# Optimization experiments

Hardware: AMD Instinct MI355X
Metric: run time of the kernel (lower is better)

Reference implementation:

```python
import jax, jax.numpy as jnp
import numpy as np

L_F, HOP, DELTA, L_S, COND, GH = 32, 16, 3, 96, 32, 64
B, T = 128, 48000


def setup_inputs() -> dict:
    key = jax.random.key(0)
    ks = jax.random.split(key, 12)
    s = 0.05
    return {
        "x": jax.random.normal(ks[0], (B, T), jnp.float32),
        # GRU (PyTorch layout): weight_ih (3H, L_S), weight_hh (3H, H)
        "W_ih": jax.random.normal(ks[1], (3 * GH, L_S), jnp.float32) * s,
        "W_hh": jax.random.normal(ks[2], (3 * GH, GH), jnp.float32) * s,
        "b_ih": jax.random.normal(ks[3], (3 * GH,), jnp.float32) * s,
        "b_hh": jax.random.normal(ks[4], (3 * GH,), jnp.float32) * s,
        # SlowBranch output projection -> cond_dim
        "W_cs": jax.random.normal(ks[5], (COND, GH), jnp.float32) * s,
        "b_cs": jax.random.normal(ks[6], (COND,), jnp.float32) * s,
        # FastEC MLP
        "W1": jax.random.normal(ks[7], (GH, L_F + COND), jnp.float32) * s,
        "b1": jax.random.normal(ks[8], (GH,), jnp.float32) * s,
        "W2": jax.random.normal(ks[9], (L_F, GH), jnp.float32) * s,
        "b2": jax.random.normal(ks[10], (L_F,), jnp.float32) * s,
    }


def reference(x, W_ih, W_hh, b_ih, b_hh, W_cs, b_cs, W1, b1, W2, b2):
    Bsz, Tlen = x.shape
    Nf = (Tlen - L_F) // HOP + 1
    win_s = DELTA * HOP * 2
    hop_s = DELTA * HOP
    Ns = (Tlen - win_s) // hop_s + 1

    f_starts = jnp.arange(Nf) * HOP                      # (Nf,)
    fast_idx = f_starts[:, None] + jnp.arange(L_F)       # (Nf, L_F)
    fast_frames = x[:, fast_idx]                         # (B, Nf, L_F)

    s_starts = jnp.arange(Ns) * hop_s
    slow_frames = x[:, s_starts[:, None] + jnp.arange(win_s)]  # (B, Ns, L_S)

    # Single-layer GRU over slow frames (PyTorch gate order r, z, n)
    def step(h, xt):
        gi = xt @ W_ih.T + b_ih                          # (B, 3H)
        gh = h @ W_hh.T + b_hh
        i_r, i_z, i_n = jnp.split(gi, 3, axis=-1)
        h_r, h_z, h_n = jnp.split(gh, 3, axis=-1)
        r = jax.nn.sigmoid(i_r + h_r)
        z = jax.nn.sigmoid(i_z + h_z)
        n = jnp.tanh(i_n + r * h_n)
        hn = (1.0 - z) * n + z * h
        return hn, hn

    h0 = jnp.zeros((Bsz, GH), x.dtype)
    _, hs = jax.lax.scan(step, h0, jnp.swapaxes(slow_frames, 0, 1))
    hs = jnp.swapaxes(hs, 0, 1)                          # (B, Ns, GH)
    c_s = hs @ W_cs.T + b_cs                             # (B, Ns, COND)

    # per-fast-frame conditioning vector (gather)
    idx = jnp.clip(jnp.arange(Nf) // DELTA - 1, 0, None)
    c = c_s[:, idx]                                      # (B, Nf, COND)

    # FastEC batched over all frames at once
    h = jnp.concatenate([fast_frames, c], axis=-1)       # (B, Nf, L_F+COND)
    h = jax.nn.relu(h @ W1.T + b1)
    y = h @ W2.T + b2                                    # (B, Nf, L_F)

    # overlap-add scatter
    out = jnp.zeros_like(x).at[:, fast_idx].add(y)
    return out
```

## Files before the change

kernel.cpp:

```cpp
#include <hip/hip_runtime.h>

constexpr int Bn  = 128;
constexpr int Tn  = 48000;
constexpr int NFn = 2999;
constexpr int NSn = 999;
constexpr int G3n = 192;
constexpr int GHn = 64;

typedef float f2 __attribute__((ext_vector_type(2)));

__global__ __launch_bounds__(192) void gi_kernel(const float* __restrict__ x,
                                                 const float* __restrict__ W_ih,
                                                 const float* __restrict__ b_ih,
                                                 float* __restrict__ GI) {
  __shared__ __align__(16) float WT[48 * 196];
  __shared__ float xs[1584];
  const int tile = blockIdx.x;
  const int b    = blockIdx.y;
  const int t0   = tile * 32;
  const int nt   = min(32, NSn - t0);
  const int tid  = threadIdx.x;

  const int span = (nt - 1) * 48 + 96;
  for (int i = tid; i < 1584; i += 192)
    xs[i] = (i < span) ? x[(size_t)b * Tn + t0 * 48 + i] : 0.0f;

  const int jq = tid % 48;
  const int tg = tid / 48;
  const int j0 = jq * 4;

  float acc[8][4];
#pragma unroll
  for (int u = 0; u < 8; ++u)
#pragma unroll
    for (int jj = 0; jj < 4; ++jj) acc[u][jj] = b_ih[j0 + jj];

  for (int half = 0; half < 2; ++half) {
    __syncthreads();
    for (int e = tid; e < 192 * 48; e += 192) {
      int j = e / 48, k = e % 48;
      WT[k * 196 + j] = W_ih[j * 96 + half * 48 + k];
    }
    __syncthreads();
    for (int k = 0; k < 48; ++k) {
      float4 w = *(const float4*)&WT[k * 196 + j0];
#pragma unroll
      for (int u = 0; u < 8; ++u) {
        float xv = xs[(tg * 8 + u) * 48 + half * 48 + k];
        acc[u][0] = fmaf(xv, w.x, acc[u][0]);
        acc[u][1] = fmaf(xv, w.y, acc[u][1]);
        acc[u][2] = fmaf(xv, w.z, acc[u][2]);
        acc[u][3] = fmaf(xv, w.w, acc[u][3]);
      }
    }
  }

#pragma unroll
  for (int u = 0; u < 8; ++u) {
    int tl = tg * 8 + u;
    if (tl < nt) {
      float4 st = make_float4(acc[u][0], acc[u][1], acc[u][2], acc[u][3]);
      *(float4*)&GI[(size_t)(b * NSn + t0 + tl) * G3n + j0] = st;
    }
  }
}

__device__ __forceinline__ float fsigmoid(float v) {
  return __fdividef(1.0f, 1.0f + __expf(-v));
}
__device__ __forceinline__ float ftanh_f(float v) {
  return 1.0f - __fdividef(2.0f, __expf(2.0f * v) + 1.0f);
}

__global__ __attribute__((amdgpu_flat_work_group_size(64, 64),
                          amdgpu_waves_per_eu(1, 1),
                          amdgpu_num_vgpr(256)))
void gru_kernel(const float* __restrict__ GI,
                const float* __restrict__ W_hh,
                const float* __restrict__ b_hh,
                float* __restrict__ hs) {
  __shared__ __align__(16) float hbuf[64];
  const int b = blockIdx.x;
  const int j = threadIdx.x;

  f2 wr2[32], wz2[32], wn2[32];
  const f2* Wr = (const f2*)(W_hh + (size_t)j * 64);
  const f2* Wz = (const f2*)(W_hh + (size_t)(j + 64) * 64);
  const f2* Wn = (const f2*)(W_hh + (size_t)(j + 128) * 64);
#pragma unroll
  for (int q = 0; q < 32; ++q) { wr2[q] = Wr[q]; wz2[q] = Wz[q]; wn2[q] = Wn[q]; }
#pragma unroll
  for (int q = 0; q < 32; ++q) {
    asm volatile("" : "+v"(wr2[q]));
    asm volatile("" : "+v"(wz2[q]));
    asm volatile("" : "+v"(wn2[q]));
  }
  const float br = b_hh[j], bz = b_hh[j + 64], bn = b_hh[j + 128];

  hbuf[j] = 0.0f;
  float hj = 0.0f;
  __builtin_amdgcn_wave_barrier();

  const float* gp = GI + (size_t)b * NSn * G3n;
  float* hsp = hs + (size_t)b * NSn * GHn;

  float pr0, pr1, pr2, pz0, pz1, pz2, pn0, pn1, pn2;
  pr0 = gp[0 * G3n + j];       pz0 = gp[0 * G3n + 64 + j];  pn0 = gp[0 * G3n + 128 + j];
  pr1 = gp[1 * G3n + j];       pz1 = gp[1 * G3n + 64 + j];  pn1 = gp[1 * G3n + 128 + j];

  for (int t = 0; t < NSn; ++t) {
    const size_t off = (size_t)min(t + 2, NSn - 1) * G3n;
    pr2 = gp[off + j];
    pz2 = gp[off + 64 + j];
    pn2 = gp[off + 128 + j];

    const f2* h2 = (const f2*)hbuf;
    f2 ar0 = {0.f, 0.f}, ar1 = {0.f, 0.f}, ar2 = {0.f, 0.f}, ar3 = {0.f, 0.f};
    f2 az0 = {0.f, 0.f}, az1 = {0.f, 0.f}, az2 = {0.f, 0.f}, az3 = {0.f, 0.f};
    f2 an0 = {0.f, 0.f}, an1 = {0.f, 0.f}, an2 = {0.f, 0.f}, an3 = {0.f, 0.f};
#pragma unroll
    for (int q = 0; q < 8; ++q) {
      f2 h0 = h2[q * 4 + 0], h1 = h2[q * 4 + 1], h2v = h2[q * 4 + 2], h3 = h2[q * 4 + 3];
      ar0 += wr2[q * 4 + 0] * h0; ar1 += wr2[q * 4 + 1] * h1;
      ar2 += wr2[q * 4 + 2] * h2v; ar3 += wr2[q * 4 + 3] * h3;
      az0 += wz2[q * 4 + 0] * h0; az1 += wz2[q * 4 + 1] * h1;
      az2 += wz2[q * 4 + 2] * h2v; az3 += wz2[q * 4 + 3] * h3;
      an0 += wn2[q * 4 + 0] * h0; an1 += wn2[q * 4 + 1] * h1;
      an2 += wn2[q * 4 + 2] * h2v; an3 += wn2[q * 4 + 3] * h3;
    }
    f2 sr = (ar0 + ar1) + (ar2 + ar3);
    f2 sz = (az0 + az1) + (az2 + az3);
    f2 sn = (an0 + an1) + (an2 + an3);

    float r = fsigmoid(pr0 + br + sr.x + sr.y);
    float z = fsigmoid(pz0 + bz + sz.x + sz.y);
    float n = ftanh_f(fmaf(r, bn + sn.x + sn.y, pn0));
    float hn = fmaf(z, hj - n, n);

    __builtin_amdgcn_wave_barrier();
    hbuf[j] = hn;
    __builtin_amdgcn_wave_barrier();
    hj = hn;
    hsp[(size_t)t * GHn + j] = hn;

    pr0 = pr1; pr1 = pr2;
    pz0 = pz1; pz1 = pz2;
    pn0 = pn1; pn1 = pn2;
  }
}

__global__ __launch_bounds__(256) void cs_kernel(const float* __restrict__ hs,
                                                 const float* __restrict__ W_cs,
                                                 const float* __restrict__ b_cs,
                                                 float* __restrict__ cs) {
  __shared__ __align__(16) float WcT[64 * 36];
  __shared__ __align__(16) float hsl[32 * 65];
  __shared__ __align__(16) float bcs[32];
  const int tile = blockIdx.x;
  const int b    = blockIdx.y;
  const int t0   = tile * 32;
  const int nt   = min(32, NSn - t0);
  const int tid  = threadIdx.x;

  for (int e = tid; e < 32 * 64; e += 256) {
    int i = e >> 6, k = e & 63;
    WcT[k * 36 + i] = W_cs[e];
  }
  for (int e = tid; e < nt * 64; e += 256) {
    int t = e >> 6, k = e & 63;
    hsl[t * 65 + k] = hs[((size_t)b * NSn + t0 + t) * GHn + k];
  }
  if (tid < 32) bcs[tid] = b_cs[tid];
  __syncthreads();

  const int oq = tid & 7;
  const int t  = tid >> 3;
  if (t < nt) {
    float4 acc = *(const float4*)&bcs[oq * 4];
    const float* hr = &hsl[t * 65];
#pragma unroll 4
    for (int k = 0; k < 64; ++k) {
      float hv = hr[k];
      float4 w = *(const float4*)&WcT[k * 36 + oq * 4];
      acc.x = fmaf(w.x, hv, acc.x);
      acc.y = fmaf(w.y, hv, acc.y);
      acc.z = fmaf(w.z, hv, acc.z);
      acc.w = fmaf(w.w, hv, acc.w);
    }
    *(float4*)&cs[((size_t)b * NSn + t0 + t) * 32 + oq * 4] = acc;
  }
}

__global__ __launch_bounds__(256) void out_kernel(const float* __restrict__ x,
                                                  const float* __restrict__ cs,
                                                  const float* __restrict__ W1,
                                                  const float* __restrict__ b1,
                                                  const float* __restrict__ W2,
                                                  const float* __restrict__ b2,
                                                  float* __restrict__ out) {
  __shared__ __align__(16) float A[33 * 65];
  __shared__ __align__(16) float W1T[64 * 68];
  __shared__ __align__(16) float W2T[64 * 36];
  __shared__ __align__(16) float h1loc[33 * 65];
  __shared__ __align__(16) float yloc[33 * 32];
  __shared__ __align__(16) float bb1[64];
  __shared__ __align__(16) float bb2[32];

  const int fb  = blockIdx.x;
  const int b   = blockIdx.y;
  const int f0  = fb * 32;
  const int nf  = min(33, NFn - f0);
  const int tid = threadIdx.x;

  for (int e = tid; e < 64 * 64; e += 256) {
    int o = e >> 6, k = e & 63;
    W1T[k * 68 + o] = W1[e];
  }
  for (int e = tid; e < 32 * 64; e += 256) {
    int o = e >> 6, k = e & 63;
    W2T[k * 36 + o] = W2[e];
  }
  if (tid < 64) bb1[tid] = b1[tid];
  if (tid < 32) bb2[tid] = b2[tid];

  for (int e = tid; e < 33 * 32; e += 256) {
    int lf = e >> 5, k = e & 31;
    int g = (f0 + lf) * 16 + k;
    A[lf * 65 + k] = (lf < nf && g < Tn) ? x[(size_t)b * Tn + g] : 0.0f;
  }
  for (int e = tid; e < 33 * 32; e += 256) {
    int lf = e >> 5, k = e & 31;
    int ts = max((f0 + lf) / 3 - 1, 0);
    A[lf * 65 + 32 + k] = (lf < nf) ? cs[((size_t)b * NSn + ts) * 32 + k] : 0.0f;
  }
  __syncthreads();

  for (int it = tid; it < 33 * 16; it += 256) {
    int lf = it >> 4, oq = it & 15;
    float4 acc = *(const float4*)&bb1[oq * 4];
    const float* ar = &A[lf * 65];
#pragma unroll 4
    for (int k = 0; k < 64; ++k) {
      float av = ar[k];
      float4 w = *(const float4*)&W1T[k * 68 + oq * 4];
      acc.x = fmaf(w.x, av, acc.x);
      acc.y = fmaf(w.y, av, acc.y);
      acc.z = fmaf(w.z, av, acc.z);
      acc.w = fmaf(w.w, av, acc.w);
    }
    acc.x = fmaxf(acc.x, 0.0f); acc.y = fmaxf(acc.y, 0.0f);
    acc.z = fmaxf(acc.z, 0.0f); acc.w = fmaxf(acc.w, 0.0f);
    *(float4*)&h1loc[lf * 65 + oq * 4] = acc;
  }
  __syncthreads();

  for (int it = tid; it < 33 * 8; it += 256) {
    int lf = it >> 3, oq = it & 7;
    float4 acc = *(const float4*)&bb2[oq * 4];
    const float* hr = &h1loc[lf * 65];
#pragma unroll 4
    for (int k = 0; k < 64; ++k) {
      float hv = hr[k];
      float4 w = *(const float4*)&W2T[k * 36 + oq * 4];
      acc.x = fmaf(w.x, hv, acc.x);
      acc.y = fmaf(w.y, hv, acc.y);
      acc.z = fmaf(w.z, hv, acc.z);
      acc.w = fmaf(w.w, hv, acc.w);
    }
    *(float4*)&yloc[lf * 32 + oq * 4] = acc;
  }
  __syncthreads();

  const int s0 = f0 * 16 + 16;
  const int s1 = min(s0 + 512, Tn);
  for (int s = s0 + tid; s < s1; s += 256) {
    int f1  = s >> 4;
    int o1  = s & 15;
    int lf1 = f1 - f0;
    float v = yloc[(lf1 - 1) * 32 + o1 + 16];
    if (lf1 < nf) v += yloc[lf1 * 32 + o1];
    out[(size_t)b * Tn + s] = v;
  }
  if (fb == 0 && tid < 16) out[(size_t)b * Tn + tid] = yloc[tid];
}

extern "C" void kernel_launch(void* const* d_in, const int* in_sizes, int n_in,
                              void* d_out, int out_size, void* d_ws, size_t ws_size,
                              hipStream_t stream) {
  const float* x    = (const float*)d_in[0];
  const float* W_ih = (const float*)d_in[1];
  const float* W_hh = (const float*)d_in[2];
  const float* b_ih = (const float*)d_in[3];
  const float* b_hh = (const float*)d_in[4];
  const float* W_cs = (const float*)d_in[5];
  const float* b_cs = (const float*)d_in[6];
  const float* W1   = (const float*)d_in[7];
  const float* b1   = (const float*)d_in[8];
  const float* W2   = (const float*)d_in[9];
  const float* b2   = (const float*)d_in[10];
  float* out = (float*)d_out;

  float* GI = (float*)d_ws;
  float* hs = GI + (size_t)Bn * NSn * G3n;
  float* cs = GI;

  gi_kernel<<<dim3(32, Bn), 192, 0, stream>>>(x, W_ih, b_ih, GI);
  gru_kernel<<<Bn, 64, 0, stream>>>(GI, W_hh, b_hh, hs);
  cs_kernel<<<dim3(32, Bn), 256, 0, stream>>>(hs, W_cs, b_cs, cs);
  out_kernel<<<dim3(94, Bn), 256, 0, stream>>>(x, cs, W1, b1, W2, b2, out);
}
```

Before: 875.7 us.

## Split GRU recurrence matvec across four waves with readlane broadcast and LDS reduction

The GRU kernel moves from one 64-thread wave per batch element to four waves, each covering a 16-wide slice of the hidden-state dot product. The hidden state is broadcast with readlane instead of a shared-memory round trip. Partial sums go through double-buffered LDS and are joined after a workgroup barrier. This cuts the serial FMA chain per timestep by four and frees registers, but adds a block-wide barrier and an LDS reduction to every step of the sequential loop.

```diff
diff --git a/kernel.cpp b/kernel.cpp
--- a/kernel.cpp
+++ b/kernel.cpp
@@ -8,6 +8,7 @@
 constexpr int GHn = 64;
 
 typedef float f2 __attribute__((ext_vector_type(2)));
+typedef float f4 __attribute__((ext_vector_type(4)));
 
 __global__ __launch_bounds__(192) void gi_kernel(const float* __restrict__ x,
                                                  const float* __restrict__ W_ih,
@@ -72,34 +73,38 @@
   return 1.0f - __fdividef(2.0f, __expf(2.0f * v) + 1.0f);
 }
 
-__global__ __attribute__((amdgpu_flat_work_group_size(64, 64),
-                          amdgpu_waves_per_eu(1, 1),
-                          amdgpu_num_vgpr(256)))
-void gru_kernel(const float* __restrict__ GI,
-                const float* __restrict__ W_hh,
-                const float* __restrict__ b_hh,
-                float* __restrict__ hs) {
-  __shared__ __align__(16) float hbuf[64];
-  const int b = blockIdx.x;
-  const int j = threadIdx.x;
-
-  f2 wr2[32], wz2[32], wn2[32];
-  const f2* Wr = (const f2*)(W_hh + (size_t)j * 64);
-  const f2* Wz = (const f2*)(W_hh + (size_t)(j + 64) * 64);
-  const f2* Wn = (const f2*)(W_hh + (size_t)(j + 128) * 64);
-#pragma unroll
-  for (int q = 0; q < 32; ++q) { wr2[q] = Wr[q]; wz2[q] = Wz[q]; wn2[q] = Wn[q]; }
-#pragma unroll
-  for (int q = 0; q < 32; ++q) {
-    asm volatile("" : "+v"(wr2[q]));
-    asm volatile("" : "+v"(wz2[q]));
-    asm volatile("" : "+v"(wn2[q]));
+#define GRU_LBAR()                                             \
+  do {                                                         \
+    asm volatile("s_waitcnt lgkmcnt(0)" ::: "memory");         \
+    __builtin_amdgcn_s_barrier();                              \
+    asm volatile("" ::: "memory");                             \
+  } while (0)
+
+__global__ __launch_bounds__(256) void gru_kernel(const float* __restrict__ GI,
+                                                  const float* __restrict__ W_hh,
+                                                  const float* __restrict__ b_hh,
+                                                  float* __restrict__ hs) {
+  __shared__ __align__(16) float parts[2][4][64][4];
+  const int tid = threadIdx.x;
+  const int wid = tid >> 6;
+  const int j   = tid & 63;
+  const int b   = blockIdx.x;
+  const int k0  = wid * 16;
+
+  f4 wr4[4], wz4[4], wn4[4];
+#pragma unroll
+  for (int q = 0; q < 4; ++q) {
+    wr4[q] = *(const f4*)&W_hh[(size_t)j * 64 + k0 + 4 * q];
+    wz4[q] = *(const f4*)&W_hh[(size_t)(j + 64) * 64 + k0 + 4 * q];
+    wn4[q] = *(const f4*)&W_hh[(size_t)(j + 128) * 64 + k0 + 4 * q];
+  }
+#pragma unroll
+  for (int q = 0; q < 4; ++q) {
+    asm volatile("" : "+v"(wr4[q]));
+    asm volatile("" : "+v"(wz4[q]));
+    asm volatile("" : "+v"(wn4[q]));
   }
   const float br = b_hh[j], bz = b_hh[j + 64], bn = b_hh[j + 128];
-
-  hbuf[j] = 0.0f;
-  float hj = 0.0f;
-  __builtin_amdgcn_wave_barrier();
 
   const float* gp = GI + (size_t)b * NSn * G3n;
   float* hsp = hs + (size_t)b * NSn * GHn;
@@ -107,6 +112,8 @@
   float pr0, pr1, pr2, pz0, pz1, pz2, pn0, pn1, pn2;
   pr0 = gp[0 * G3n + j];       pz0 = gp[0 * G3n + 64 + j];  pn0 = gp[0 * G3n + 128 + j];
   pr1 = gp[1 * G3n + j];       pz1 = gp[1 * G3n + 64 + j];  pn1 = gp[1 * G3n + 128 + j];
+
+  float hn = 0.0f;
 
   for (int t = 0; t < NSn; ++t) {
     const size_t off = (size_t)min(t + 2, NSn - 1) * G3n;
@@ -114,34 +121,49 @@
     pz2 = gp[off + 64 + j];
     pn2 = gp[off + 128 + j];
 
-    const f2* h2 = (const f2*)hbuf;
-    f2 ar0 = {0.f, 0.f}, ar1 = {0.f, 0.f}, ar2 = {0.f, 0.f}, ar3 = {0.f, 0.f};
-    f2 az0 = {0.f, 0.f}, az1 = {0.f, 0.f}, az2 = {0.f, 0.f}, az3 = {0.f, 0.f};
-    f2 an0 = {0.f, 0.f}, an1 = {0.f, 0.f}, an2 = {0.f, 0.f}, an3 = {0.f, 0.f};
-#pragma unroll
-    for (int q = 0; q < 8; ++q) {
-      f2 h0 = h2[q * 4 + 0], h1 = h2[q * 4 + 1], h2v = h2[q * 4 + 2], h3 = h2[q * 4 + 3];
-      ar0 += wr2[q * 4 + 0] * h0; ar1 += wr2[q * 4 + 1] * h1;
-      ar2 += wr2[q * 4 + 2] * h2v; ar3 += wr2[q * 4 + 3] * h3;
-      az0 += wz2[q * 4 + 0] * h0; az1 += wz2[q * 4 + 1] * h1;
-      az2 += wz2[q * 4 + 2] * h2v; az3 += wz2[q * 4 + 3] * h3;
-      an0 += wn2[q * 4 + 0] * h0; an1 += wn2[q * 4 + 1] * h1;
-      an2 += wn2[q * 4 + 2] * h2v; an3 += wn2[q * 4 + 3] * h3;
-    }
-    f2 sr = (ar0 + ar1) + (ar2 + ar3);
-    f2 sz = (az0 + az1) + (az2 + az3);
-    f2 sn = (an0 + an1) + (an2 + an3);
-
-    float r = fsigmoid(pr0 + br + sr.x + sr.y);
-    float z = fsigmoid(pz0 + bz + sz.x + sz.y);
-    float n = ftanh_f(fmaf(r, bn + sn.x + sn.y, pn0));
-    float hn = fmaf(z, hj - n, n);
-
-    __builtin_amdgcn_wave_barrier();
-    hbuf[j] = hn;
-    __builtin_amdgcn_wave_barrier();
-    hj = hn;
-    hsp[(size_t)t * GHn + j] = hn;
+    float sh[16];
+#pragma unroll
+    for (int m = 0; m < 16; ++m)
+      sh[m] = __uint_as_float(
+          __builtin_amdgcn_readlane(__float_as_uint(hn), k0 + m));
+
+    float ar0 = 0.f, ar1 = 0.f, ar2 = 0.f, ar3 = 0.f;
+    float az0 = 0.f, az1 = 0.f, az2 = 0.f, az3 = 0.f;
+    float an0 = 0.f, an1 = 0.f, an2 = 0.f, an3 = 0.f;
+#pragma unroll
+    for (int q = 0; q < 4; ++q) {
+      float h0 = sh[4 * q + 0], h1 = sh[4 * q + 1];
+      float h2v = sh[4 * q + 2], h3 = sh[4 * q + 3];
+      ar0 = fmaf(wr4[q][0], h0, ar0); ar1 = fmaf(wr4[q][1], h1, ar1);
+      ar2 = fmaf(wr4[q][2], h2v, ar2); ar3 = fmaf(wr4[q][3], h3, ar3);
+      az0 = fmaf(wz4[q][0], h0, az0); az1 = fmaf(wz4[q][1], h1, az1);
+      az2 = fmaf(wz4[q][2], h2v, az2); az3 = fmaf(wz4[q][3], h3, az3);
+      an0 = fmaf(wn4[q][0], h0, an0); an1 = fmaf(wn4[q][1], h1, an1);
+      an2 = fmaf(wn4[q][2], h2v, an2); an3 = fmaf(wn4[q][3], h3, an3);
+    }
+    f4 pv;
+    pv[0] = (ar0 + ar1) + (ar2 + ar3);
+    pv[1] = (az0 + az1) + (az2 + az3);
+    pv[2] = (an0 + an1) + (an2 + an3);
+    pv[3] = 0.f;
+    *(f4*)&parts[t & 1][wid][j][0] = pv;
+
+    GRU_LBAR();
+
+    const f4 p0 = *(const f4*)&parts[t & 1][0][j][0];
+    const f4 p1 = *(const f4*)&parts[t & 1][1][j][0];
+    const f4 p2 = *(const f4*)&parts[t & 1][2][j][0];
+    const f4 p3 = *(const f4*)&parts[t & 1][3][j][0];
+    float sr = (p0[0] + p1[0]) + (p2[0] + p3[0]);
+    float sz = (p0[1] + p1[1]) + (p2[1] + p3[1]);
+    float sn = (p0[2] + p1[2]) + (p2[2] + p3[2]);
+
+    float r = fsigmoid(pr0 + br + sr);
+    float z = fsigmoid(pz0 + bz + sz);
+    float n = ftanh_f(fmaf(r, bn + sn, pn0));
+    hn = fmaf(z, hn - n, n);
+
+    if (wid == 0) hsp[(size_t)t * GHn + j] = hn;
 
     pr0 = pr1; pr1 = pr2;
     pz0 = pz1; pz1 = pz2;
@@ -305,7 +327,7 @@
   float* cs = GI;
 
   gi_kernel<<<dim3(32, Bn), 192, 0, stream>>>(x, W_ih, b_ih, GI);
-  gru_kernel<<<Bn, 64, 0, stream>>>(GI, W_hh, b_hh, hs);
+  gru_kernel<<<Bn, 256, 0, stream>>>(GI, W_hh, b_hh, hs);
   cs_kernel<<<dim3(32, Bn), 256, 0, stream>>>(hs, W_cs, b_cs, cs);
   out_kernel<<<dim3(94, Bn), 256, 0, stream>>>(x, cs, W1, b1, W2, b2, out);
 }
```

Result: slower. 1.080 ms (+23.3%).

## Hold MLP weights in registers and split K across threads in out_kernel

Applied to the files above, without the earlier changes.

The FastEC MLP kernel stops staging transposed W1/W2 in shared memory. Each thread now loads a 4x32 slice of weights straight from global memory into registers and computes a half-K partial dot product for several frames. A shared-memory reduction then sums the two halves and applies the bias and ReLU. The aim is to cut LDS traffic and shared-memory weight loads, at the cost of very high register use (launch_bounds min-blocks 1), which may limit occupancy, plus extra syncs for the partial sums.

```diff
diff --git a/kernel.cpp b/kernel.cpp
--- a/kernel.cpp
+++ b/kernel.cpp
@@ -8,6 +8,7 @@
 constexpr int GHn = 64;
 
 typedef float f2 __attribute__((ext_vector_type(2)));
+typedef float f4 __attribute__((ext_vector_type(4)));
 
 __global__ __launch_bounds__(192) void gi_kernel(const float* __restrict__ x,
                                                  const float* __restrict__ W_ih,
@@ -191,17 +192,17 @@
   }
 }
 
-__global__ __launch_bounds__(256) void out_kernel(const float* __restrict__ x,
-                                                  const float* __restrict__ cs,
-                                                  const float* __restrict__ W1,
-                                                  const float* __restrict__ b1,
-                                                  const float* __restrict__ W2,
-                                                  const float* __restrict__ b2,
-                                                  float* __restrict__ out) {
-  __shared__ __align__(16) float A[33 * 65];
-  __shared__ __align__(16) float W1T[64 * 68];
-  __shared__ __align__(16) float W2T[64 * 36];
-  __shared__ __align__(16) float h1loc[33 * 65];
+__global__ __launch_bounds__(256, 1) void out_kernel(const float* __restrict__ x,
+                                                     const float* __restrict__ cs,
+                                                     const float* __restrict__ W1,
+                                                     const float* __restrict__ b1,
+                                                     const float* __restrict__ W2,
+                                                     const float* __restrict__ b2,
+                                                     float* __restrict__ out) {
+  __shared__ __align__(16) float A[33 * 68];
+  __shared__ __align__(16) float P[2][33][64];
+  __shared__ __align__(16) float h1loc[33 * 68];
+  __shared__ __align__(16) float P2[2][33][32];
   __shared__ __align__(16) float yloc[33 * 32];
   __shared__ __align__(16) float bb1[64];
   __shared__ __align__(16) float bb2[32];
@@ -212,62 +213,115 @@
   const int nf  = min(33, NFn - f0);
   const int tid = threadIdx.x;
 
-  for (int e = tid; e < 64 * 64; e += 256) {
-    int o = e >> 6, k = e & 63;
-    W1T[k * 68 + o] = W1[e];
-  }
-  for (int e = tid; e < 32 * 64; e += 256) {
-    int o = e >> 6, k = e & 63;
-    W2T[k * 36 + o] = W2[e];
-  }
+  const int oq  = tid & 15;
+  const int kh  = (tid >> 4) & 1;
+  const int lfp = tid >> 5;
+
+  f4 w1r[4][8];
+#pragma unroll
+  for (int r = 0; r < 4; ++r)
+#pragma unroll
+    for (int i = 0; i < 8; ++i)
+      w1r[r][i] = *(const f4*)&W1[(size_t)(oq * 4 + r) * 64 + kh * 32 + 4 * i];
+
   if (tid < 64) bb1[tid] = b1[tid];
   if (tid < 32) bb2[tid] = b2[tid];
 
   for (int e = tid; e < 33 * 32; e += 256) {
     int lf = e >> 5, k = e & 31;
     int g = (f0 + lf) * 16 + k;
-    A[lf * 65 + k] = (lf < nf && g < Tn) ? x[(size_t)b * Tn + g] : 0.0f;
+    A[lf * 68 + k] = (lf < nf && g < Tn) ? x[(size_t)b * Tn + g] : 0.0f;
   }
   for (int e = tid; e < 33 * 32; e += 256) {
     int lf = e >> 5, k = e & 31;
     int ts = max((f0 + lf) / 3 - 1, 0);
-    A[lf * 65 + 32 + k] = (lf < nf) ? cs[((size_t)b * NSn + ts) * 32 + k] : 0.0f;
-  }
-  __syncthreads();
-
-  for (int it = tid; it < 33 * 16; it += 256) {
-    int lf = it >> 4, oq = it & 15;
-    float4 acc = *(const float4*)&bb1[oq * 4];
-    const float* ar = &A[lf * 65];
-#pragma unroll 4
-    for (int k = 0; k < 64; ++k) {
-      float av = ar[k];
-      float4 w = *(const float4*)&W1T[k * 68 + oq * 4];
-      acc.x = fmaf(w.x, av, acc.x);
-      acc.y = fmaf(w.y, av, acc.y);
-      acc.z = fmaf(w.z, av, acc.z);
-      acc.w = fmaf(w.w, av, acc.w);
-    }
-    acc.x = fmaxf(acc.x, 0.0f); acc.y = fmaxf(acc.y, 0.0f);
-    acc.z = fmaxf(acc.z, 0.0f); acc.w = fmaxf(acc.w, 0.0f);
-    *(float4*)&h1loc[lf * 65 + oq * 4] = acc;
-  }
-  __syncthreads();
-
-  for (int it = tid; it < 33 * 8; it += 256) {
-    int lf = it >> 3, oq = it & 7;
-    float4 acc = *(const float4*)&bb2[oq * 4];
-    const float* hr = &h1loc[lf * 65];
-#pragma unroll 4
-    for (int k = 0; k < 64; ++k) {
-      float hv = hr[k];
-      float4 w = *(const float4*)&W2T[k * 36 + oq * 4];
-      acc.x = fmaf(w.x, hv, acc.x);
-      acc.y = fmaf(w.y, hv, acc.y);
-      acc.z = fmaf(w.z, hv, acc.z);
-      acc.w = fmaf(w.w, hv, acc.w);
-    }
-    *(float4*)&yloc[lf * 32 + oq * 4] = acc;
+    A[lf * 68 + 32 + k] = (lf < nf) ? cs[((size_t)b * NSn + ts) * 32 + k] : 0.0f;
+  }
+  __syncthreads();
+
+#pragma unroll
+  for (int m = 0; m < 5; ++m) {
+    const int lf = lfp + 8 * m;
+    if (lf < 33) {
+      const f4* ar = (const f4*)&A[lf * 68 + kh * 32];
+      f4 av[8];
+#pragma unroll
+      for (int i = 0; i < 8; ++i) av[i] = ar[i];
+      float a0 = 0.f, a1 = 0.f, a2 = 0.f, a3 = 0.f;
+#pragma unroll
+      for (int i = 0; i < 8; ++i) {
+#pragma unroll
+        for (int c = 0; c < 4; ++c) {
+          const float avc = av[i][c];
+          a0 = fmaf(w1r[0][i][c], avc, a0);
+          a1 = fmaf(w1r[1][i][c], avc, a1);
+          a2 = fmaf(w1r[2][i][c], avc, a2);
+          a3 = fmaf(w1r[3][i][c], avc, a3);
+        }
+      }
+      f4 pv = {a0, a1, a2, a3};
+      *(f4*)&P[kh][lf][oq * 4] = pv;
+    }
+  }
+  __syncthreads();
+
+  for (int e = tid; e < 33 * 16; e += 256) {
+    const int lf = e >> 4, q = e & 15;
+    f4 p0 = *(const f4*)&P[0][lf][q * 4];
+    f4 p1 = *(const f4*)&P[1][lf][q * 4];
+    f4 bq = *(const f4*)&bb1[q * 4];
+    f4 s = p0 + p1 + bq;
+#pragma unroll
+    for (int c = 0; c < 4; ++c) s[c] = fmaxf(s[c], 0.f);
+    *(f4*)&h1loc[lf * 68 + q * 4] = s;
+  }
+  __syncthreads();
+
+  const int oq2  = tid & 7;
+  const int kh2  = (tid >> 3) & 1;
+  const int lfp2 = tid >> 4;
+
+  asm volatile("" ::: "memory");
+  f4 w2r[4][8];
+#pragma unroll
+  for (int r = 0; r < 4; ++r)
+#pragma unroll
+    for (int i = 0; i < 8; ++i)
+      w2r[r][i] = *(const f4*)&W2[(size_t)(oq2 * 4 + r) * 64 + kh2 * 32 + 4 * i];
+
+#pragma unroll
+  for (int m = 0; m < 3; ++m) {
+    const int lf = lfp2 + 16 * m;
+    if (lf < 33) {
+      const f4* hr = (const f4*)&h1loc[lf * 68 + kh2 * 32];
+      f4 hv[8];
+#pragma unroll
+      for (int i = 0; i < 8; ++i) hv[i] = hr[i];
+      float a0 = 0.f, a1 = 0.f, a2 = 0.f, a3 = 0.f;
+#pragma unroll
+      for (int i = 0; i < 8; ++i) {
+#pragma unroll
+        for (int c = 0; c < 4; ++c) {
+          const float hvc = hv[i][c];
+          a0 = fmaf(w2r[0][i][c], hvc, a0);
+          a1 = fmaf(w2r[1][i][c], hvc, a1);
+          a2 = fmaf(w2r[2][i][c], hvc, a2);
+          a3 = fmaf(w2r[3][i][c], hvc, a3);
+        }
+      }
+      f4 pv = {a0, a1, a2, a3};
+      *(f4*)&P2[kh2][lf][oq2 * 4] = pv;
+    }
+  }
+  __syncthreads();
+
+  for (int e = tid; e < 33 * 8; e += 256) {
+    const int lf = e >> 3, q = e & 7;
+    f4 p0 = *(const f4*)&P2[0][lf][q * 4];
+    f4 p1 = *(const f4*)&P2[1][lf][q * 4];
+    f4 bq = *(const f4*)&bb2[q * 4];
+    f4 s = p0 + p1 + bq;
+    *(f4*)&yloc[lf * 32 + q * 4] = s;
   }
   __syncthreads();
 
```

Result: slower. 1.288 ms (+47.1%).

## Overlap fast-branch x·W1 projection with GRU recurrence in one grid

Applied to the files above, without the earlier changes.

Splits the first FastEC layer algebraically into a frame part (x·W1[:, :32]) and a conditioning part (c·W1[:, 32:]). The frame part is computed by extra blocks launched in the same grid as the latency-bound GRU, so they fill idle CUs during the sequential recurrence. The conditioning part is folded into a per-slow-step vector d, so the output kernel only needs add, ReLU and the W2 projection. This adds a large U workspace buffer and depends on the workspace being big enough, otherwise it falls back to the old path.

```diff
diff --git a/kernel.cpp b/kernel.cpp
--- a/kernel.cpp
+++ b/kernel.cpp
@@ -8,6 +8,7 @@
 constexpr int GHn = 64;
 
 typedef float f2 __attribute__((ext_vector_type(2)));
+typedef float f4 __attribute__((ext_vector_type(4)));
 
 __global__ __launch_bounds__(192) void gi_kernel(const float* __restrict__ x,
                                                  const float* __restrict__ W_ih,
@@ -72,6 +73,77 @@
   return 1.0f - __fdividef(2.0f, __expf(2.0f * v) + 1.0f);
 }
 
+__device__ __forceinline__ void gru_body(const float* __restrict__ GI,
+                                         const float* __restrict__ W_hh,
+                                         const float* __restrict__ b_hh,
+                                         float* __restrict__ hs,
+                                         float* hbuf, int b, int j) {
+  f2 wr2[32], wz2[32], wn2[32];
+  const f2* Wr = (const f2*)(W_hh + (size_t)j * 64);
+  const f2* Wz = (const f2*)(W_hh + (size_t)(j + 64) * 64);
+  const f2* Wn = (const f2*)(W_hh + (size_t)(j + 128) * 64);
+#pragma unroll
+  for (int q = 0; q < 32; ++q) { wr2[q] = Wr[q]; wz2[q] = Wz[q]; wn2[q] = Wn[q]; }
+#pragma unroll
+  for (int q = 0; q < 32; ++q) {
+    asm volatile("" : "+v"(wr2[q]));
+    asm volatile("" : "+v"(wz2[q]));
+    asm volatile("" : "+v"(wn2[q]));
+  }
+  const float br = b_hh[j], bz = b_hh[j + 64], bn = b_hh[j + 128];
+
+  hbuf[j] = 0.0f;
+  float hj = 0.0f;
+  __builtin_amdgcn_wave_barrier();
+
+  const float* gp = GI + (size_t)b * NSn * G3n;
+  float* hsp = hs + (size_t)b * NSn * GHn;
+
+  float pr0, pr1, pr2, pz0, pz1, pz2, pn0, pn1, pn2;
+  pr0 = gp[0 * G3n + j];       pz0 = gp[0 * G3n + 64 + j];  pn0 = gp[0 * G3n + 128 + j];
+  pr1 = gp[1 * G3n + j];       pz1 = gp[1 * G3n + 64 + j];  pn1 = gp[1 * G3n + 128 + j];
+
+  for (int t = 0; t < NSn; ++t) {
+    const size_t off = (size_t)min(t + 2, NSn - 1) * G3n;
+    pr2 = gp[off + j];
+    pz2 = gp[off + 64 + j];
+    pn2 = gp[off + 128 + j];
+
+    const f2* h2 = (const f2*)hbuf;
+    f2 ar0 = {0.f, 0.f}, ar1 = {0.f, 0.f}, ar2 = {0.f, 0.f}, ar3 = {0.f, 0.f};
+    f2 az0 = {0.f, 0.f}, az1 = {0.f, 0.f}, az2 = {0.f, 0.f}, az3 = {0.f, 0.f};
+    f2 an0 = {0.f, 0.f}, an1 = {0.f, 0.f}, an2 = {0.f, 0.f}, an3 = {0.f, 0.f};
+#pragma unroll
+    for (int q = 0; q < 8; ++q) {
+      f2 h0 = h2[q * 4 + 0], h1 = h2[q * 4 + 1], h2v = h2[q * 4 + 2], h3 = h2[q * 4 + 3];
+      ar0 += wr2[q * 4 + 0] * h0; ar1 += wr2[q * 4 + 1] * h1;
+      ar2 += wr2[q * 4 + 2] * h2v; ar3 += wr2[q * 4 + 3] * h3;
+      az0 += wz2[q * 4 + 0] * h0; az1 += wz2[q * 4 + 1] * h1;
+      az2 += wz2[q * 4 + 2] * h2v; az3 += wz2[q * 4 + 3] * h3;
+      an0 += wn2[q * 4 + 0] * h0; an1 += wn2[q * 4 + 1] * h1;
+      an2 += wn2[q * 4 + 2] * h2v; an3 += wn2[q * 4 + 3] * h3;
+    }
+    f2 sr = (ar0 + ar1) + (ar2 + ar3);
+    f2 sz = (az0 + az1) + (az2 + az3);
+    f2 sn = (an0 + an1) + (an2 + an3);
+
+    float r = fsigmoid(pr0 + br + sr.x + sr.y);
+    float z = fsigmoid(pz0 + bz + sz.x + sz.y);
+    float n = ftanh_f(fmaf(r, bn + sn.x + sn.y, pn0));
+    float hn = fmaf(z, hj - n, n);
+
+    __builtin_amdgcn_wave_barrier();
+    hbuf[j] = hn;
+    __builtin_amdgcn_wave_barrier();
+    hj = hn;
+    hsp[(size_t)t * GHn + j] = hn;
+
+    pr0 = pr1; pr1 = pr2;
+    pz0 = pz1; pz1 = pz2;
+    pn0 = pn1; pn1 = pn2;
+  }
+}
+
 __global__ __attribute__((amdgpu_flat_work_group_size(64, 64),
                           amdgpu_waves_per_eu(1, 1),
                           amdgpu_num_vgpr(256)))
@@ -80,72 +152,135 @@
                 const float* __restrict__ b_hh,
                 float* __restrict__ hs) {
   __shared__ __align__(16) float hbuf[64];
-  const int b = blockIdx.x;
-  const int j = threadIdx.x;
-
-  f2 wr2[32], wz2[32], wn2[32];
-  const f2* Wr = (const f2*)(W_hh + (size_t)j * 64);
-  const f2* Wz = (const f2*)(W_hh + (size_t)(j + 64) * 64);
-  const f2* Wn = (const f2*)(W_hh + (size_t)(j + 128) * 64);
-#pragma unroll
-  for (int q = 0; q < 32; ++q) { wr2[q] = Wr[q]; wz2[q] = Wz[q]; wn2[q] = Wn[q]; }
-#pragma unroll
-  for (int q = 0; q < 32; ++q) {
-    asm volatile("" : "+v"(wr2[q]));
-    asm volatile("" : "+v"(wz2[q]));
-    asm volatile("" : "+v"(wn2[q]));
-  }
-  const float br = b_hh[j], bz = b_hh[j + 64], bn = b_hh[j + 128];
-
-  hbuf[j] = 0.0f;
-  float hj = 0.0f;
-  __builtin_amdgcn_wave_barrier();
-
-  const float* gp = GI + (size_t)b * NSn * G3n;
-  float* hsp = hs + (size_t)b * NSn * GHn;
-
-  float pr0, pr1, pr2, pz0, pz1, pz2, pn0, pn1, pn2;
-  pr0 = gp[0 * G3n + j];       pz0 = gp[0 * G3n + 64 + j];  pn0 = gp[0 * G3n + 128 + j];
-  pr1 = gp[1 * G3n + j];       pz1 = gp[1 * G3n + 64 + j];  pn1 = gp[1 * G3n + 128 + j];
-
-  for (int t = 0; t < NSn; ++t) {
-    const size_t off = (size_t)min(t + 2, NSn - 1) * G3n;
-    pr2 = gp[off + j];
-    pz2 = gp[off + 64 + j];
-    pn2 = gp[off + 128 + j];
-
-    const f2* h2 = (const f2*)hbuf;
-    f2 ar0 = {0.f, 0.f}, ar1 = {0.f, 0.f}, ar2 = {0.f, 0.f}, ar3 = {0.f, 0.f};
-    f2 az0 = {0.f, 0.f}, az1 = {0.f, 0.f}, az2 = {0.f, 0.f}, az3 = {0.f, 0.f};
-    f2 an0 = {0.f, 0.f}, an1 = {0.f, 0.f}, an2 = {0.f, 0.f}, an3 = {0.f, 0.f};
-#pragma unroll
-    for (int q = 0; q < 8; ++q) {
-      f2 h0 = h2[q * 4 + 0], h1 = h2[q * 4 + 1], h2v = h2[q * 4 + 2], h3 = h2[q * 4 + 3];
-      ar0 += wr2[q * 4 + 0] * h0; ar1 += wr2[q * 4 + 1] * h1;
-      ar2 += wr2[q * 4 + 2] * h2v; ar3 += wr2[q * 4 + 3] * h3;
-      az0 += wz2[q * 4 + 0] * h0; az1 += wz2[q * 4 + 1] * h1;
-      az2 += wz2[q * 4 + 2] * h2v; az3 += wz2[q * 4 + 3] * h3;
-      an0 += wn2[q * 4 + 0] * h0; an1 += wn2[q * 4 + 1] * h1;
-      an2 += wn2[q * 4 + 2] * h2v; an3 += wn2[q * 4 + 3] * h3;
-    }
-    f2 sr = (ar0 + ar1) + (ar2 + ar3);
-    f2 sz = (az0 + az1) + (az2 + az3);
-    f2 sn = (an0 + an1) + (an2 + an3);
-
-    float r = fsigmoid(pr0 + br + sr.x + sr.y);
-    float z = fsigmoid(pz0 + bz + sz.x + sz.y);
-    float n = ftanh_f(fmaf(r, bn + sn.x + sn.y, pn0));
-    float hn = fmaf(z, hj - n, n);
-
-    __builtin_amdgcn_wave_barrier();
-    hbuf[j] = hn;
-    __builtin_amdgcn_wave_barrier();
-    hj = hn;
-    hsp[(size_t)t * GHn + j] = hn;
-
-    pr0 = pr1; pr1 = pr2;
-    pz0 = pz1; pz1 = pz2;
-    pn0 = pn1; pn1 = pn2;
+  gru_body(GI, W_hh, b_hh, hs, hbuf, blockIdx.x, threadIdx.x);
+}
+
+constexpr int UCHUNK = 125;
+constexpr int NCH    = 24;
+
+__global__ __attribute__((amdgpu_flat_work_group_size(64, 64),
+                          amdgpu_waves_per_eu(1, 1),
+                          amdgpu_num_vgpr(256)))
+void fat_kernel(const float* __restrict__ GI,
+                const float* __restrict__ W_hh,
+                const float* __restrict__ b_hh,
+                float* __restrict__ hs,
+                const float* __restrict__ x,
+                const float* __restrict__ W1,
+                const float* __restrict__ b1,
+                float* __restrict__ U) {
+  __shared__ __align__(16) float hbuf[64];
+  __shared__ __align__(16) float xs[UCHUNK * 16 + 16];
+  const int tid = threadIdx.x;
+
+  if (blockIdx.x < Bn) {
+    gru_body(GI, W_hh, b_hh, hs, hbuf, blockIdx.x, tid);
+    return;
+  }
+
+  const int ub = blockIdx.x - Bn;
+  const int b  = ub / NCH;
+  const int ch = ub % NCH;
+  const int fA = ch * UCHUNK;
+  const int fE = min(fA + UCHUNK, NFn);
+  const int o  = tid;
+
+  const int nsamp = (fE - fA - 1) * 16 + 32;
+  for (int i = tid; i < nsamp; i += 64)
+    xs[i] = x[(size_t)b * Tn + fA * 16 + i];
+
+  f4 w1f[8];
+#pragma unroll
+  for (int i = 0; i < 8; ++i)
+    w1f[i] = *(const f4*)&W1[(size_t)o * 64 + 4 * i];
+  const float bo = b1[o];
+  __syncthreads();
+
+  float* Up = U + ((size_t)b * NFn) * GHn + o;
+  for (int f = fA; f < fE; ++f) {
+    const f4* xq = (const f4*)&xs[(f - fA) * 16];
+    float a0 = bo, a1 = 0.f, a2 = 0.f, a3 = 0.f;
+#pragma unroll
+    for (int i = 0; i < 8; ++i) {
+      f4 xv = xq[i];
+      a0 = fmaf(xv[0], w1f[i][0], a0);
+      a1 = fmaf(xv[1], w1f[i][1], a1);
+      a2 = fmaf(xv[2], w1f[i][2], a2);
+      a3 = fmaf(xv[3], w1f[i][3], a3);
+    }
+    Up[(size_t)f * GHn] = (a0 + a1) + (a2 + a3);
+  }
+}
+
+__global__ __launch_bounds__(256) void d_kernel(const float* __restrict__ hs,
+                                                const float* __restrict__ W_cs,
+                                                const float* __restrict__ b_cs,
+                                                const float* __restrict__ W1,
+                                                float* __restrict__ d) {
+  __shared__ __align__(16) float WcT[64 * 36];
+  __shared__ __align__(16) float W1cT[32 * 68];
+  __shared__ __align__(16) float hsl[32 * 65];
+  __shared__ __align__(16) float cloc[32 * 36];
+  __shared__ __align__(16) float bcs[32];
+  const int tile = blockIdx.x;
+  const int b    = blockIdx.y;
+  const int t0   = tile * 32;
+  const int nt   = min(32, NSn - t0);
+  const int tid  = threadIdx.x;
+
+  for (int e = tid; e < 32 * 64; e += 256) {
+    int i = e >> 6, k = e & 63;
+    WcT[k * 36 + i] = W_cs[e];
+  }
+  for (int e = tid; e < 64 * 32; e += 256) {
+    int o = e >> 5, i = e & 31;
+    W1cT[i * 68 + o] = W1[(size_t)o * 64 + 32 + i];
+  }
+  for (int e = tid; e < nt * 64; e += 256) {
+    int t = e >> 6, k = e & 63;
+    hsl[t * 65 + k] = hs[((size_t)b * NSn + t0 + t) * GHn + k];
+  }
+  if (tid < 32) bcs[tid] = b_cs[tid];
+  __syncthreads();
+
+  {
+    const int iq = tid & 7;
+    const int t  = tid >> 3;
+    if (t < nt) {
+      float4 acc = *(const float4*)&bcs[iq * 4];
+      const float* hr = &hsl[t * 65];
+#pragma unroll 4
+      for (int k = 0; k < 64; ++k) {
+        float hv = hr[k];
+        float4 w = *(const float4*)&WcT[k * 36 + iq * 4];
+        acc.x = fmaf(w.x, hv, acc.x);
+        acc.y = fmaf(w.y, hv, acc.y);
+        acc.z = fmaf(w.z, hv, acc.z);
+        acc.w = fmaf(w.w, hv, acc.w);
+      }
+      *(float4*)&cloc[t * 36 + iq * 4] = acc;
+    }
+  }
+  __syncthreads();
+
+  for (int it = tid; it < 32 * 16; it += 256) {
+    const int oq = it & 15;
+    const int t  = it >> 4;
+    if (t < nt) {
+      float a0 = 0.f, a1 = 0.f, a2 = 0.f, a3 = 0.f;
+      const float* cr = &cloc[t * 36];
+#pragma unroll 4
+      for (int i = 0; i < 32; ++i) {
+        float cv = cr[i];
+        float4 w = *(const float4*)&W1cT[i * 68 + oq * 4];
+        a0 = fmaf(w.x, cv, a0);
+        a1 = fmaf(w.y, cv, a1);
+        a2 = fmaf(w.z, cv, a2);
+        a3 = fmaf(w.w, cv, a3);
+      }
+      float4 st = make_float4(a0, a1, a2, a3);
+      *(float4*)&d[((size_t)b * NSn + t0 + t) * GHn + oq * 4] = st;
+    }
   }
 }
 
@@ -189,6 +324,82 @@
     }
     *(float4*)&cs[((size_t)b * NSn + t0 + t) * 32 + oq * 4] = acc;
   }
+}
+
+__global__ __launch_bounds__(256) void out2_kernel(const float* __restrict__ U,
+                                                   const float* __restrict__ d,
+                                                   const float* __restrict__ W2,
+                                                   const float* __restrict__ b2,
+                                                   float* __restrict__ out) {
+  __shared__ __align__(16) float h1loc[33 * 68];
+  __shared__ __align__(16) float W2T[64 * 36];
+  __shared__ __align__(16) float yloc[33 * 32];
+  __shared__ __align__(16) float dloc[12][68];
+  __shared__ __align__(16) float bb2[32];
+
+  const int fb  = blockIdx.x;
+  const int b   = blockIdx.y;
+  const int f0  = fb * 32;
+  const int nf  = min(33, NFn - f0);
+  const int tid = threadIdx.x;
+  const int ts0 = max(f0 / 3 - 1, 0);
+
+  for (int e = tid; e < 32 * 64; e += 256) {
+    int o = e >> 6, k = e & 63;
+    W2T[k * 36 + o] = W2[e];
+  }
+  if (tid < 32) bb2[tid] = b2[tid];
+  for (int e = tid; e < 12 * 64; e += 256) {
+    int ti = e >> 6, o = e & 63;
+    int ts = min(ts0 + ti, NSn - 1);
+    dloc[ti][o] = d[((size_t)b * NSn + ts) * GHn + o];
+  }
+  __syncthreads();
+
+  for (int it = tid; it < 33 * 16; it += 256) {
+    const int lf = it >> 4, oq = it & 15;
+    const int f  = f0 + lf;
+    f4 s = {0.f, 0.f, 0.f, 0.f};
+    if (f < NFn) {
+      f4 u  = *(const f4*)&U[((size_t)b * NFn + f) * GHn + oq * 4];
+      const int ti = max(f / 3 - 1, 0) - ts0;
+      f4 dv = *(const f4*)&dloc[ti][oq * 4];
+      s = u + dv;
+#pragma unroll
+      for (int c = 0; c < 4; ++c) s[c] = fmaxf(s[c], 0.f);
+    }
+    *(f4*)&h1loc[lf * 68 + oq * 4] = s;
+  }
+  __syncthreads();
+
+  for (int it = tid; it < 33 * 8; it += 256) {
+    const int lf = it >> 3, oq = it & 7;
+    float4 acc = *(const float4*)&bb2[oq * 4];
+    const float* hr = &h1loc[lf * 68];
+#pragma unroll 4
+    for (int k = 0; k < 64; ++k) {
+      float hv = hr[k];
+      float4 w = *(const float4*)&W2T[k * 36 + oq * 4];
+      acc.x = fmaf(w.x, hv, acc.x);
+      acc.y = fmaf(w.y, hv, acc.y);
+      acc.z = fmaf(w.z, hv, acc.z);
+      acc.w = fmaf(w.w, hv, acc.w);
+    }
+    *(float4*)&yloc[lf * 32 + oq * 4] = acc;
+  }
+  __syncthreads();
+
+  const int s0 = f0 * 16 + 16;
+  const int s1 = min(s0 + 512, Tn);
+  for (int s = s0 + tid; s < s1; s += 256) {
+    int f1  = s >> 4;
+    int o1  = s & 15;
+    int lf1 = f1 - f0;
+    float v = yloc[(lf1 - 1) * 32 + o1 + 16];
+    if (lf1 < nf) v += yloc[lf1 * 32 + o1];
+    out[(size_t)b * Tn + s] = v;
+  }
+  if (fb == 0 && tid < 16) out[(size_t)b * Tn + tid] = yloc[tid];
 }
 
 __global__ __launch_bounds__(256) void out_kernel(const float* __restrict__ x,
@@ -300,12 +511,26 @@
   const float* b2   = (const float*)d_in[10];
   float* out = (float*)d_out;
 
+  const size_t giN = (size_t)Bn * NSn * G3n;
+  const size_t hsN = (size_t)Bn * NSn * GHn;
+  const size_t uN  = (size_t)Bn * NFn * GHn;
+
   float* GI = (float*)d_ws;
-  float* hs = GI + (size_t)Bn * NSn * G3n;
-  float* cs = GI;
+  float* hs = GI + giN;
 
   gi_kernel<<<dim3(32, Bn), 192, 0, stream>>>(x, W_ih, b_ih, GI);
-  gru_kernel<<<Bn, 64, 0, stream>>>(GI, W_hh, b_hh, hs);
-  cs_kernel<<<dim3(32, Bn), 256, 0, stream>>>(hs, W_cs, b_cs, cs);
-  out_kernel<<<dim3(94, Bn), 256, 0, stream>>>(x, cs, W1, b1, W2, b2, out);
-}
+
+  if (ws_size >= (giN + hsN + uN) * sizeof(float)) {
+    float* U = hs + hsN;
+    float* d = GI;
+    fat_kernel<<<Bn + Bn * NCH, 64, 0, stream>>>(GI, W_hh, b_hh, hs,
+                                                 x, W1, b1, U);
+    d_kernel<<<dim3(32, Bn), 256, 0, stream>>>(hs, W_cs, b_cs, W1, d);
+    out2_kernel<<<dim3(94, Bn), 256, 0, stream>>>(U, d, W2, b2, out);
+  } else {
+    float* cs = GI;
+    gru_kernel<<<Bn, 64, 0, stream>>>(GI, W_hh, b_hh, hs);
+    cs_kernel<<<dim3(32, Bn), 256, 0, stream>>>(hs, W_cs, b_cs, cs);
+    out_kernel<<<dim3(94, Bn), 256, 0, stream>>>(x, cs, W1, b1, W2, b2, out);
+  }
+}
```

Measured after the change: 771.6 us. -11.9%, faster.
